# Kernel tuning notes

Hardware: AMD Instinct MI355X
Metric: run time of the kernel (lower is better)

The kernel has to match this reference:

```python
import jax, jax.numpy as jnp
import numpy as np

N_NODES = 50000
N_EDGES = 800000
D = 128
DEPTH = 3


def setup_inputs() -> dict:
    key = jax.random.key(0)
    ks = jax.random.split(key, 10)
    s = 1.0 / np.sqrt(D)
    return {
        "h": jax.random.normal(ks[0], (N_NODES, D), dtype=jnp.float32),
        "src": jax.random.randint(ks[1], (N_EDGES,), 0, N_NODES, dtype=jnp.int32),
        "dst": jax.random.randint(ks[2], (N_EDGES,), 0, N_NODES, dtype=jnp.int32),
        "W_in1": jax.random.normal(ks[3], (D, D), dtype=jnp.float32) * s,
        "b_in1": jnp.zeros((D,), dtype=jnp.float32),
        "W_in2": jax.random.normal(ks[4], (D, D), dtype=jnp.float32) * s,
        "b_in2": jnp.zeros((D,), dtype=jnp.float32),
        "W_self": jax.random.normal(ks[5], (DEPTH, D, D), dtype=jnp.float32) * s,
        "b_self": jnp.zeros((DEPTH, D), dtype=jnp.float32),
        "W_neigh": jax.random.normal(ks[6], (DEPTH, D, D), dtype=jnp.float32) * s,
    }


def _mean_aggregate(h, src, dst, n_nodes):
    # gather source features along edges, sum into destination, divide by in-degree
    msg = h[src]                                             # [E, D]
    summed = jax.ops.segment_sum(msg, dst, num_segments=n_nodes)  # [N, D]
    deg = jax.ops.segment_sum(jnp.ones_like(dst, dtype=h.dtype), dst,
                              num_segments=n_nodes)          # [N]
    return summed / jnp.maximum(deg, 1.0)[:, None]


def reference(h, src, dst, W_in1, b_in1, W_in2, b_in2, W_self, b_self, W_neigh):
    n_nodes = h.shape[0]
    # fc_in: Linear -> tanh -> Linear
    h = jnp.tanh(h @ W_in1 + b_in1) @ W_in2 + b_in2
    # stacked SAGEConv(mean) layers with SiLU between layers
    for i in range(DEPTH):
        h_neigh = _mean_aggregate(h, src, dst, n_nodes)
        h = h @ W_self[i] + b_self[i] + h_neigh @ W_neigh[i]
        if i < DEPTH - 1:
            h = jax.nn.silu(h)
    return jnp.tanh(h)
```

## Files before the change

### kernel.cpp

```cpp
#include <hip/hip_runtime.h>
#include <stdint.h>

#define DD 128
#define LDSROW 136

typedef __attribute__((ext_vector_type(8))) short short8;
typedef __attribute__((ext_vector_type(4))) float float4v;

__device__ __forceinline__ unsigned short f2bf(float f) {
  unsigned u = __float_as_uint(f);
  unsigned r = u + 0x7fffu + ((u >> 16) & 1u);
  return (unsigned short)(r >> 16);
}
__device__ __forceinline__ unsigned pack2(float a, float b) {
  return (unsigned)f2bf(a) | ((unsigned)f2bf(b) << 16);
}
__device__ __forceinline__ float2 unpack2(unsigned p) {
  float2 r;
  r.x = __uint_as_float(p << 16);
  r.y = __uint_as_float(p & 0xffff0000u);
  return r;
}

__global__ __launch_bounds__(256) void k_deg_prep(const int* __restrict__ dst, int* deg,
                                                  unsigned short* __restrict__ erank,
                                                  int e, int eb,
                                                  const float* __restrict__ W1, const float* __restrict__ W2,
                                                  const float* __restrict__ Wself, const float* __restrict__ Wneigh,
                                                  unsigned* __restrict__ wfrag) {
  int b = blockIdx.x;
  if (b < eb) {
    int i = b * 256 + threadIdx.x;
    if (i < e) erank[i] = (unsigned short)atomicAdd(&deg[dst[i]], 1);
  } else {
    int gid = (b - eb) * 256 + threadIdx.x;
    int m = gid >> 13;
    int r = gid & 8191;
    int p = r & 3;
    int lane = (r >> 2) & 63;
    int t = (r >> 8) & 3;
    int c = r >> 10;
    const float* W;
    if (m == 0) W = W1;
    else if (m == 1) W = W2;
    else if (m < 5) W = Wself + (size_t)(m - 2) * DD * DD;
    else W = Wneigh + (size_t)(m - 5) * DD * DD;
    int n = c * 16 + (lane & 15);
    int k = t * 32 + (lane >> 4) * 8 + 2 * p;
    wfrag[gid] = pack2(W[(size_t)k * DD + n], W[(size_t)(k + 1) * DD + n]);
  }
}

__global__ __launch_bounds__(1024) void k_scan1(const int* __restrict__ deg, int* __restrict__ incl,
                                                int* __restrict__ bsum, int n) {
  __shared__ int sh[1024];
  int t = threadIdx.x;
  int i = blockIdx.x * 1024 + t;
  int v = (i < n) ? deg[i] : 0;
  sh[t] = v;
  __syncthreads();
#pragma unroll
  for (int off = 1; off < 1024; off <<= 1) {
    int add = (t >= off) ? sh[t - off] : 0;
    __syncthreads();
    sh[t] += add;
    __syncthreads();
  }
  if (i < n) incl[i] = sh[t];
  if (t == 1023) bsum[blockIdx.x] = sh[1023];
}

__global__ __launch_bounds__(1024) void k_scan3(const int* __restrict__ deg, const int* __restrict__ incl,
                                                const int* __restrict__ bsum, int* __restrict__ rowstart,
                                                int n, int nb) {
  __shared__ int sboff;
  int t = threadIdx.x;
  if (t < 64) {
    int orig = (t < nb) ? bsum[t] : 0;
    int v = orig;
#pragma unroll
    for (int off = 1; off < 64; off <<= 1) {
      int u = __shfl_up(v, off);
      if (t >= off) v += u;
    }
    if (t == (int)blockIdx.x) sboff = v - orig;
  }
  __syncthreads();
  int i = blockIdx.x * 1024 + t;
  if (i >= n) return;
  int d = deg[i];
  int excl = sboff + incl[i] - d;
  rowstart[i] = excl;
  if (i == n - 1) rowstart[n] = excl + d;
}

__global__ __launch_bounds__(256) void k_fill_fc(const int* __restrict__ src, const int* __restrict__ dst,
                                                 const unsigned short* __restrict__ erank,
                                                 const int* __restrict__ rowstart,
                                                 unsigned short* __restrict__ esrc, int e, int gb,
                                                 const float* __restrict__ h,
                                                 const uint4* __restrict__ wf1, const uint4* __restrict__ wf2,
                                                 const float* __restrict__ b1, const float* __restrict__ b2,
                                                 unsigned short* __restrict__ outbf, int n) {
  __shared__ unsigned short sT[64 * LDSROW];
  int b = blockIdx.x;
  if (b >= gb) {
    int i = (b - gb) * 256 + threadIdx.x;
    if (i < e) {
      int d = dst[i];
      int p = rowstart[d] + (int)erank[i];
      esrc[p] = (unsigned short)src[i];
    }
    return;
  }
  int tid = threadIdx.x, w = tid >> 6, lane = tid & 63;
  int q = lane >> 4, nn = lane & 15;
  int r0 = (b * 4 + w) * 16;
  int rr = r0 + nn; if (rr >= n) rr = n - 1;
  short8 a[4];
  {
    const float* X = h + (size_t)rr * DD;
#pragma unroll
    for (int t = 0; t < 4; ++t) {
      int k0 = t * 32 + q * 8;
      float4 f0 = *(const float4*)&X[k0];
      float4 f1 = *(const float4*)&X[k0 + 4];
      uint4 u;
      u.x = pack2(f0.x, f0.y); u.y = pack2(f0.z, f0.w);
      u.z = pack2(f1.x, f1.y); u.w = pack2(f1.z, f1.w);
      a[t] = __builtin_bit_cast(short8, u);
    }
  }
  float4v acc[8];
#pragma unroll
  for (int c = 0; c < 8; ++c) acc[c] = (float4v){0.f, 0.f, 0.f, 0.f};
#pragma unroll
  for (int c = 0; c < 8; ++c) {
#pragma unroll
    for (int t = 0; t < 4; ++t) {
      short8 bb = __builtin_bit_cast(short8, wf1[(c * 4 + t) * 64 + lane]);
      acc[c] = __builtin_amdgcn_mfma_f32_16x16x32_bf16(a[t], bb, acc[c], 0, 0, 0);
    }
  }
#pragma unroll
  for (int c = 0; c < 8; ++c) {
    float bc = b1[c * 16 + nn];
#pragma unroll
    for (int g = 0; g < 4; ++g) {
      int lr = w * 16 + q * 4 + g;
      sT[lr * LDSROW + c * 16 + nn] = f2bf(tanhf(acc[c][g] + bc));
    }
  }
  __syncthreads();
  short8 a2[4];
#pragma unroll
  for (int t = 0; t < 4; ++t) {
    const uint4* p = (const uint4*)&sT[(w * 16 + nn) * LDSROW + (t * 4 + q) * 8];
    a2[t] = __builtin_bit_cast(short8, *p);
  }
  float4v acc2[8];
#pragma unroll
  for (int c = 0; c < 8; ++c) acc2[c] = (float4v){0.f, 0.f, 0.f, 0.f};
#pragma unroll
  for (int c = 0; c < 8; ++c) {
#pragma unroll
    for (int t = 0; t < 4; ++t) {
      short8 bb = __builtin_bit_cast(short8, wf2[(c * 4 + t) * 64 + lane]);
      acc2[c] = __builtin_amdgcn_mfma_f32_16x16x32_bf16(a2[t], bb, acc2[c], 0, 0, 0);
    }
  }
#pragma unroll
  for (int c = 0; c < 8; ++c) {
    float bc = b2[c * 16 + nn];
#pragma unroll
    for (int g = 0; g < 4; ++g) {
      int row = r0 + q * 4 + g;
      if (row < n) outbf[(size_t)row * DD + c * 16 + nn] = f2bf(acc2[c][g] + bc);
    }
  }
}

template <int ACT, bool OUTF32>
__global__ __launch_bounds__(256) void k_layer16(const uint4* __restrict__ X,
                                                 const int* __restrict__ rowstart,
                                                 const unsigned short* __restrict__ esrc,
                                                 const uint4* __restrict__ wfs, const uint4* __restrict__ wfn,
                                                 const float* __restrict__ bias, void* __restrict__ outp, int n) {
  __shared__ unsigned short sG[16 * LDSROW];
  int tid = threadIdx.x;
  int grp = tid >> 4, nn = tid & 15;
  int r0 = blockIdx.x * 16;
  int r = r0 + grp;
  if (r < n) {
    int beg = rowstart[r];
    int cnt = rowstart[r + 1] - beg;
    float acc[8];
#pragma unroll
    for (int i = 0; i < 8; ++i) acc[i] = 0.f;
    int base = 0;
    for (; base + 8 <= cnt; base += 8) {
      int j0 = beg + base;
      int s0 = esrc[j0], s1 = esrc[j0 + 1], s2 = esrc[j0 + 2], s3 = esrc[j0 + 3];
      int s4 = esrc[j0 + 4], s5 = esrc[j0 + 5], s6 = esrc[j0 + 6], s7 = esrc[j0 + 7];
      uint4 v0 = X[(size_t)s0 * 16 + nn];
      uint4 v1 = X[(size_t)s1 * 16 + nn];
      uint4 v2 = X[(size_t)s2 * 16 + nn];
      uint4 v3 = X[(size_t)s3 * 16 + nn];
      uint4 v4 = X[(size_t)s4 * 16 + nn];
      uint4 v5 = X[(size_t)s5 * 16 + nn];
      uint4 v6 = X[(size_t)s6 * 16 + nn];
      uint4 v7 = X[(size_t)s7 * 16 + nn];
      const unsigned* u0 = (const unsigned*)&v0;
      const unsigned* u1 = (const unsigned*)&v1;
      const unsigned* u2 = (const unsigned*)&v2;
      const unsigned* u3 = (const unsigned*)&v3;
      const unsigned* u4 = (const unsigned*)&v4;
      const unsigned* u5 = (const unsigned*)&v5;
      const unsigned* u6 = (const unsigned*)&v6;
      const unsigned* u7 = (const unsigned*)&v7;
#pragma unroll
      for (int k = 0; k < 4; ++k) {
        float2 f0 = unpack2(u0[k]), f1 = unpack2(u1[k]);
        float2 f2 = unpack2(u2[k]), f3 = unpack2(u3[k]);
        float2 f4 = unpack2(u4[k]), f5 = unpack2(u5[k]);
        float2 f6 = unpack2(u6[k]), f7 = unpack2(u7[k]);
        acc[2 * k]     += ((f0.x + f1.x) + (f2.x + f3.x)) + ((f4.x + f5.x) + (f6.x + f7.x));
        acc[2 * k + 1] += ((f0.y + f1.y) + (f2.y + f3.y)) + ((f4.y + f5.y) + (f6.y + f7.y));
      }
    }
    if (base + 4 <= cnt) {
      int j0 = beg + base;
      int s0 = esrc[j0], s1 = esrc[j0 + 1], s2 = esrc[j0 + 2], s3 = esrc[j0 + 3];
      uint4 v0 = X[(size_t)s0 * 16 + nn];
      uint4 v1 = X[(size_t)s1 * 16 + nn];
      uint4 v2 = X[(size_t)s2 * 16 + nn];
      uint4 v3 = X[(size_t)s3 * 16 + nn];
      const unsigned* u0 = (const unsigned*)&v0;
      const unsigned* u1 = (const unsigned*)&v1;
      const unsigned* u2 = (const unsigned*)&v2;
      const unsigned* u3 = (const unsigned*)&v3;
#pragma unroll
      for (int k = 0; k < 4; ++k) {
        float2 f0 = unpack2(u0[k]), f1 = unpack2(u1[k]);
        float2 f2 = unpack2(u2[k]), f3 = unpack2(u3[k]);
        acc[2 * k]     += (f0.x + f1.x) + (f2.x + f3.x);
        acc[2 * k + 1] += (f0.y + f1.y) + (f2.y + f3.y);
      }
      base += 4;
    }
    for (; base < cnt; ++base) {
      int s = esrc[beg + base];
      uint4 v = X[(size_t)s * 16 + nn];
      const unsigned* u = (const unsigned*)&v;
#pragma unroll
      for (int k = 0; k < 4; ++k) {
        float2 f = unpack2(u[k]);
        acc[2 * k] += f.x;
        acc[2 * k + 1] += f.y;
      }
    }
    float inv = 1.0f / (float)(cnt > 1 ? cnt : 1);
    uint4 o;
    o.x = pack2(acc[0] * inv, acc[1] * inv);
    o.y = pack2(acc[2] * inv, acc[3] * inv);
    o.z = pack2(acc[4] * inv, acc[5] * inv);
    o.w = pack2(acc[6] * inv, acc[7] * inv);
    *(uint4*)&sG[grp * LDSROW + nn * 8] = o;
  }
  __syncthreads();
  int w = tid >> 6, lane = tid & 63;
  int q = lane >> 4, nn16 = lane & 15;
  int rr = r0 + nn16; if (rr >= n) rr = n - 1;
  short8 a[4], gf[4];
  {
    const uint4* Xr = X + (size_t)rr * 16;
#pragma unroll
    for (int t = 0; t < 4; ++t) {
      a[t] = __builtin_bit_cast(short8, Xr[t * 4 + q]);
      gf[t] = __builtin_bit_cast(short8, *(const uint4*)&sG[nn16 * LDSROW + (t * 4 + q) * 8]);
    }
  }
  float4v acc2[2];
#pragma unroll
  for (int cc = 0; cc < 2; ++cc) acc2[cc] = (float4v){0.f, 0.f, 0.f, 0.f};
#pragma unroll
  for (int cc = 0; cc < 2; ++cc) {
    int c = 2 * w + cc;
#pragma unroll
    for (int t = 0; t < 4; ++t) {
      short8 b = __builtin_bit_cast(short8, wfs[(c * 4 + t) * 64 + lane]);
      acc2[cc] = __builtin_amdgcn_mfma_f32_16x16x32_bf16(a[t], b, acc2[cc], 0, 0, 0);
    }
#pragma unroll
    for (int t = 0; t < 4; ++t) {
      short8 b = __builtin_bit_cast(short8, wfn[(c * 4 + t) * 64 + lane]);
      acc2[cc] = __builtin_amdgcn_mfma_f32_16x16x32_bf16(gf[t], b, acc2[cc], 0, 0, 0);
    }
  }
#pragma unroll
  for (int cc = 0; cc < 2; ++cc) {
    int c = 2 * w + cc;
    float bc = bias[c * 16 + nn16];
#pragma unroll
    for (int gg = 0; gg < 4; ++gg) {
      int row = r0 + q * 4 + gg;
      if (row < n) {
        float v = acc2[cc][gg] + bc;
        if (ACT == 1) v = tanhf(v);
        else v = v / (1.f + __expf(-v));
        if (OUTF32) ((float*)outp)[(size_t)row * DD + c * 16 + nn16] = v;
        else ((unsigned short*)outp)[(size_t)row * DD + c * 16 + nn16] = f2bf(v);
      }
    }
  }
}

extern "C" void kernel_launch(void* const* d_in, const int* in_sizes, int n_in,
                              void* d_out, int out_size, void* d_ws, size_t ws_size,
                              hipStream_t stream) {
  const float* h_in = (const float*)d_in[0];
  const int* src    = (const int*)d_in[1];
  const int* dst    = (const int*)d_in[2];
  const float* W1   = (const float*)d_in[3];
  const float* b1   = (const float*)d_in[4];
  const float* W2   = (const float*)d_in[5];
  const float* b2   = (const float*)d_in[6];
  const float* Wself  = (const float*)d_in[7];
  const float* bself  = (const float*)d_in[8];
  const float* Wneigh = (const float*)d_in[9];
  const int N = in_sizes[0] / DD;
  const int E = in_sizes[1];
  float* out = (float*)d_out;

  char* ws = (char*)d_ws;
  size_t off = 0;
  auto alloc = [&](size_t bytes) -> char* {
    char* p = ws + off;
    off = (off + bytes + 255) & ~(size_t)255;
    return p;
  };
  unsigned* wfrag = (unsigned*)alloc(8 * 32768);
  unsigned* actA  = (unsigned*)alloc((size_t)N * 64 * 4);
  unsigned* actB  = (unsigned*)alloc((size_t)N * 64 * 4);
  unsigned short* esrc  = (unsigned short*)alloc((size_t)E * 2);
  unsigned short* erank = (unsigned short*)alloc((size_t)E * 2);
  int* degi     = (int*)alloc((size_t)N * 4);
  int* rowstart = (int*)alloc((size_t)(N + 1) * 4);
  int* incl     = (int*)alloc((size_t)N * 4);
  int* bsum     = (int*)alloc(65 * 4);

  hipMemsetAsync(degi, 0, (size_t)N * 4, stream);
  const int eb = (E + 255) / 256;
  const int nb = (N + 1023) / 1024;
  k_deg_prep<<<eb + 256, 256, 0, stream>>>(dst, degi, erank, E, eb, W1, W2, Wself, Wneigh, wfrag);
  k_scan1<<<nb, 1024, 0, stream>>>(degi, incl, bsum, N);
  k_scan3<<<nb, 1024, 0, stream>>>(degi, incl, bsum, rowstart, N, nb);

  const int gb = (N + 63) / 64;
  const int lb = (N + 15) / 16;
  const uint4* wf = (const uint4*)wfrag;

  k_fill_fc<<<gb + eb, 256, 0, stream>>>(src, dst, erank, rowstart, esrc, E, gb,
                                         h_in, wf + 0 * 2048, wf + 1 * 2048, b1, b2,
                                         (unsigned short*)actB, N);

  const unsigned* cur = actB;
  unsigned* nxt = actA;
  for (int l = 0; l < 3; ++l) {
    const uint4* wsF = wf + (size_t)(2 + l) * 2048;
    const uint4* wnF = wf + (size_t)(5 + l) * 2048;
    const float* bs = bself + (size_t)l * DD;
    if (l < 2) {
      k_layer16<2, false><<<lb, 256, 0, stream>>>((const uint4*)cur, rowstart, esrc, wsF, wnF, bs, nxt, N);
      const unsigned* tmp = cur;
      cur = nxt;
      nxt = (unsigned*)tmp;
    } else {
      k_layer16<1, true><<<lb, 256, 0, stream>>>((const uint4*)cur, rowstart, esrc, wsF, wnF, bs, out, N);
    }
  }
}
```

Before: 289.6 us.

## Fuse scan kernels via last-block pattern and predicate aggregation tail

Merges the two prefix-scan kernels into one: each block scans its chunk, bumps an atomic counter, and the last block to finish computes the block offsets and writes all rowstart values. This removes one kernel launch and its inter-kernel gap, but the final pass now runs on a single 1024-thread block. The aggregation remainder loop is also replaced by a single predicated 8-wide gather that uses clamped indices and zero weights, cutting serial tail iterations at the cost of some redundant loads.

```diff
diff --git a/kernel.cpp b/kernel.cpp
--- a/kernel.cpp
+++ b/kernel.cpp
@@ -51,9 +51,13 @@
   }
 }
 
-__global__ __launch_bounds__(1024) void k_scan1(const int* __restrict__ deg, int* __restrict__ incl,
-                                                int* __restrict__ bsum, int n) {
+__global__ __launch_bounds__(1024) void k_scan_all(const int* __restrict__ deg, int* __restrict__ incl,
+                                                   int* __restrict__ bsum, int* __restrict__ rowstart,
+                                                   int* donecnt, int n, int nb) {
   __shared__ int sh[1024];
+  __shared__ int isLast;
+  __shared__ int boff[64];
+  __shared__ int shTotal;
   int t = threadIdx.x;
   int i = blockIdx.x * 1024 + t;
   int v = (i < n) ? deg[i] : 0;
@@ -68,30 +72,31 @@
   }
   if (i < n) incl[i] = sh[t];
   if (t == 1023) bsum[blockIdx.x] = sh[1023];
-}
-
-__global__ __launch_bounds__(1024) void k_scan3(const int* __restrict__ deg, const int* __restrict__ incl,
-                                                const int* __restrict__ bsum, int* __restrict__ rowstart,
-                                                int n, int nb) {
-  __shared__ int sboff;
-  int t = threadIdx.x;
+  __threadfence();
+  __syncthreads();
+  if (t == 0) {
+    int old = atomicAdd(donecnt, 1);
+    isLast = (old == nb - 1);
+  }
+  __syncthreads();
+  if (!isLast) return;
+  __threadfence();
   if (t < 64) {
     int orig = (t < nb) ? bsum[t] : 0;
-    int v = orig;
+    int v2 = orig;
 #pragma unroll
     for (int off = 1; off < 64; off <<= 1) {
-      int u = __shfl_up(v, off);
-      if (t >= off) v += u;
-    }
-    if (t == (int)blockIdx.x) sboff = v - orig;
-  }
-  __syncthreads();
-  int i = blockIdx.x * 1024 + t;
-  if (i >= n) return;
-  int d = deg[i];
-  int excl = sboff + incl[i] - d;
-  rowstart[i] = excl;
-  if (i == n - 1) rowstart[n] = excl + d;
+      int u = __shfl_up(v2, off);
+      if (t >= off) v2 += u;
+    }
+    boff[t] = v2 - orig;
+    if (t == nb - 1) shTotal = v2;
+  }
+  __syncthreads();
+  for (int ii = t; ii < n; ii += 1024) {
+    rowstart[ii] = boff[ii >> 10] + incl[ii] - deg[ii];
+  }
+  if (t == 0) rowstart[n] = shTotal;
 }
 
 __global__ __launch_bounds__(256) void k_fill_fc(const int* __restrict__ src, const int* __restrict__ dst,
@@ -228,35 +233,49 @@
         acc[2 * k + 1] += ((f0.y + f1.y) + (f2.y + f3.y)) + ((f4.y + f5.y) + (f6.y + f7.y));
       }
     }
-    if (base + 4 <= cnt) {
+    if (base < cnt) {
+      int last = beg + cnt - 1;
       int j0 = beg + base;
-      int s0 = esrc[j0], s1 = esrc[j0 + 1], s2 = esrc[j0 + 2], s3 = esrc[j0 + 3];
+      int i1 = j0 + 1 <= last ? j0 + 1 : last;
+      int i2 = j0 + 2 <= last ? j0 + 2 : last;
+      int i3 = j0 + 3 <= last ? j0 + 3 : last;
+      int i4 = j0 + 4 <= last ? j0 + 4 : last;
+      int i5 = j0 + 5 <= last ? j0 + 5 : last;
+      int i6 = j0 + 6 <= last ? j0 + 6 : last;
+      int i7 = j0 + 7 <= last ? j0 + 7 : last;
+      float w1 = (base + 1 < cnt) ? 1.f : 0.f;
+      float w2 = (base + 2 < cnt) ? 1.f : 0.f;
+      float w3 = (base + 3 < cnt) ? 1.f : 0.f;
+      float w4 = (base + 4 < cnt) ? 1.f : 0.f;
+      float w5 = (base + 5 < cnt) ? 1.f : 0.f;
+      float w6 = (base + 6 < cnt) ? 1.f : 0.f;
+      float w7 = (base + 7 < cnt) ? 1.f : 0.f;
+      int s0 = esrc[j0], s1 = esrc[i1], s2 = esrc[i2], s3 = esrc[i3];
+      int s4 = esrc[i4], s5 = esrc[i5], s6 = esrc[i6], s7 = esrc[i7];
       uint4 v0 = X[(size_t)s0 * 16 + nn];
       uint4 v1 = X[(size_t)s1 * 16 + nn];
       uint4 v2 = X[(size_t)s2 * 16 + nn];
       uint4 v3 = X[(size_t)s3 * 16 + nn];
+      uint4 v4 = X[(size_t)s4 * 16 + nn];
+      uint4 v5 = X[(size_t)s5 * 16 + nn];
+      uint4 v6 = X[(size_t)s6 * 16 + nn];
+      uint4 v7 = X[(size_t)s7 * 16 + nn];
       const unsigned* u0 = (const unsigned*)&v0;
       const unsigned* u1 = (const unsigned*)&v1;
       const unsigned* u2 = (const unsigned*)&v2;
       const unsigned* u3 = (const unsigned*)&v3;
+      const unsigned* u4 = (const unsigned*)&v4;
+      const unsigned* u5 = (const unsigned*)&v5;
+      const unsigned* u6 = (const unsigned*)&v6;
+      const unsigned* u7 = (const unsigned*)&v7;
 #pragma unroll
       for (int k = 0; k < 4; ++k) {
         float2 f0 = unpack2(u0[k]), f1 = unpack2(u1[k]);
         float2 f2 = unpack2(u2[k]), f3 = unpack2(u3[k]);
-        acc[2 * k]     += (f0.x + f1.x) + (f2.x + f3.x);
-        acc[2 * k + 1] += (f0.y + f1.y) + (f2.y + f3.y);
-      }
-      base += 4;
-    }
-    for (; base < cnt; ++base) {
-      int s = esrc[beg + base];
-      uint4 v = X[(size_t)s * 16 + nn];
-      const unsigned* u = (const unsigned*)&v;
-#pragma unroll
-      for (int k = 0; k < 4; ++k) {
-        float2 f = unpack2(u[k]);
-        acc[2 * k] += f.x;
-        acc[2 * k + 1] += f.y;
+        float2 f4 = unpack2(u4[k]), f5 = unpack2(u5[k]);
+        float2 f6 = unpack2(u6[k]), f7 = unpack2(u7[k]);
+        acc[2 * k]     += ((f0.x + w1 * f1.x) + (w2 * f2.x + w3 * f3.x)) + ((w4 * f4.x + w5 * f5.x) + (w6 * f6.x + w7 * f7.x));
+        acc[2 * k + 1] += ((f0.y + w1 * f1.y) + (w2 * f2.y + w3 * f3.y)) + ((w4 * f4.y + w5 * f5.y) + (w6 * f6.y + w7 * f7.y));
       }
     }
     float inv = 1.0f / (float)(cnt > 1 ? cnt : 1);
@@ -344,17 +363,18 @@
   unsigned* actB  = (unsigned*)alloc((size_t)N * 64 * 4);
   unsigned short* esrc  = (unsigned short*)alloc((size_t)E * 2);
   unsigned short* erank = (unsigned short*)alloc((size_t)E * 2);
-  int* degi     = (int*)alloc((size_t)N * 4);
+  int* degdc    = (int*)alloc(((size_t)N + 64) * 4);
+  int* degi     = degdc;
+  int* donecnt  = degdc + N;
   int* rowstart = (int*)alloc((size_t)(N + 1) * 4);
   int* incl     = (int*)alloc((size_t)N * 4);
   int* bsum     = (int*)alloc(65 * 4);
 
-  hipMemsetAsync(degi, 0, (size_t)N * 4, stream);
+  hipMemsetAsync(degdc, 0, ((size_t)N + 64) * 4, stream);
   const int eb = (E + 255) / 256;
   const int nb = (N + 1023) / 1024;
   k_deg_prep<<<eb + 256, 256, 0, stream>>>(dst, degi, erank, E, eb, W1, W2, Wself, Wneigh, wfrag);
-  k_scan1<<<nb, 1024, 0, stream>>>(degi, incl, bsum, N);
-  k_scan3<<<nb, 1024, 0, stream>>>(degi, incl, bsum, rowstart, N, nb);
+  k_scan_all<<<nb, 1024, 0, stream>>>(degi, incl, bsum, rowstart, donecnt, N, nb);
 
   const int gb = (N + 63) / 64;
   const int lb = (N + 15) / 16;
```

Result: slower. 297.9 us (+2.9%).
